# Kernel tuning notes

Hardware: AMD Instinct MI355X
Metric: run time of the kernel (lower is better)

The kernel has to match this reference:

```python
import jax, jax.numpy as jnp
import numpy as np

N_NODES = 200000
N_EDGES = 6400000
N_GRAPHS = 512
DIM_IN = 128
HID = 32
BN_EPS = 1e-5


def _gin(x, src, dst, w1, b1, w2, b2):
    # GINConv with eps=0: MLP(x + sum_{j in N(i)} x_j)
    agg = jax.ops.segment_sum(x[src], dst, num_segments=N_NODES)
    h = x + agg
    h = jnp.maximum(h @ w1 + b1, 0.0)
    return h @ w2 + b2


def _bn(x, gamma, beta):
    # BatchNorm1d, training mode: batch stats, biased variance
    m = jnp.mean(x, axis=0)
    v = jnp.var(x, axis=0)
    return gamma * (x - m) * jax.lax.rsqrt(v + BN_EPS) + beta


def setup_inputs() -> dict:
    key = jax.random.key(0)
    ks = jax.random.split(key, 20)
    s = 0.1
    inp = {
        "x": jax.random.normal(ks[0], (N_NODES, DIM_IN), jnp.float32),
        "edge_index": jax.random.randint(ks[1], (2, N_EDGES), 0, N_NODES, jnp.int32),
        "batch": jnp.sort(jax.random.randint(ks[2], (N_NODES,), 0, N_GRAPHS, jnp.int32)),
        "e0_w1": s * jax.random.normal(ks[3], (DIM_IN, HID), jnp.float32),
        "e0_b1": s * jax.random.normal(ks[4], (HID,), jnp.float32),
        "e0_w2": s * jax.random.normal(ks[5], (HID, HID), jnp.float32),
        "e0_b2": s * jax.random.normal(ks[6], (HID,), jnp.float32),
        "enc_w1": s * jax.random.normal(ks[7], (4, HID, HID), jnp.float32),
        "enc_b1": s * jax.random.normal(ks[8], (4, HID), jnp.float32),
        "enc_w2": s * jax.random.normal(ks[9], (4, HID, HID), jnp.float32),
        "enc_b2": s * jax.random.normal(ks[10], (4, HID), jnp.float32),
        "enc_gamma": jnp.ones((5, HID), jnp.float32),
        "enc_beta": jnp.zeros((5, HID), jnp.float32),
        "dec_w1": s * jax.random.normal(ks[11], (5, HID, HID), jnp.float32),
        "dec_b1": s * jax.random.normal(ks[12], (5, HID), jnp.float32),
        "dec_w2": s * jax.random.normal(ks[13], (4, HID, HID), jnp.float32),
        "dec_b2": s * jax.random.normal(ks[14], (4, HID), jnp.float32),
        "dec_w2_last": s * jax.random.normal(ks[15], (HID, DIM_IN), jnp.float32),
        "dec_b2_last": s * jax.random.normal(ks[16], (DIM_IN,), jnp.float32),
        "dec_gamma": jnp.ones((4, HID), jnp.float32),
        "dec_beta": jnp.zeros((4, HID), jnp.float32),
    }
    return inp


def reference(x, edge_index, batch,
              e0_w1, e0_b1, e0_w2, e0_b2,
              enc_w1, enc_b1, enc_w2, enc_b2, enc_gamma, enc_beta,
              dec_w1, dec_b1, dec_w2, dec_b2, dec_w2_last, dec_b2_last,
              dec_gamma, dec_beta):
    src, dst = edge_index[0], edge_index[1]

    # ----- Encoder: 5 GIN layers, ReLU then BN, collect per-layer reps -----
    xs = []
    h = jnp.maximum(_gin(x, src, dst, e0_w1, e0_b1, e0_w2, e0_b2), 0.0)
    h = _bn(h, enc_gamma[0], enc_beta[0])
    xs.append(h)
    for i in range(4):
        h = jnp.maximum(_gin(h, src, dst, enc_w1[i], enc_b1[i], enc_w2[i], enc_b2[i]), 0.0)
        h = _bn(h, enc_gamma[i + 1], enc_beta[i + 1])
        xs.append(h)
    encoded_rep = h

    # ----- Decoder: 5 GIN layers, ReLU; BN on all but last -----
    d = encoded_rep
    for i in range(5):
        w2 = dec_w2[i] if i < 4 else dec_w2_last
        b2 = dec_b2[i] if i < 4 else dec_b2_last
        d = jnp.maximum(_gin(d, src, dst, dec_w1[i], dec_b1[i], w2, b2), 0.0)
        if i < 4:
            d = _bn(d, dec_gamma[i], dec_beta[i])
    decoded_rep = d

    # ----- Global add pool of each encoder layer output, concat -----
    xpool = [jax.ops.segment_sum(xi, batch, num_segments=N_GRAPHS) for xi in xs]
    global_rep = jnp.concatenate(xpool, axis=1)  # [G, 5*32]

    return encoded_rep, decoded_rep, global_rep
```

## Files before the change

kernel.cpp:

```cpp
#include <hip/hip_runtime.h>
#include <hip/hip_bf16.h>
#include <hip/hip_fp16.h>
#include <string.h>

#define N_NODES  200000
#define N_EDGES  6400000
#define N_GRAPHS 512
#define DIM_IN   128
#define HID      32
#define BN_EPS   1e-5f

#define CHUNK    2048
#define NCHUNKS  98

typedef const float* fp;

__device__ __forceinline__ unsigned short f2h(float f) {
    __half h = __float2half(f);
    unsigned short u; __builtin_memcpy(&u, &h, 2); return u;
}
__device__ __forceinline__ float2 h2f2(unsigned int u) {
    __half2 h; __builtin_memcpy(&h, &u, 4);
    return __half22float2(h);
}


__global__ __launch_bounds__(256) void k_hist2(const int* __restrict__ dst,
                                               int* __restrict__ deg) {
    __shared__ int lh[12500];
    const int grp = blockIdx.x & 15;
    const int blk = blockIdx.x >> 4;
    const int lo = grp * 12500;
    for (int j = threadIdx.x; j < 12500; j += 256) lh[j] = 0;
    __syncthreads();
    const int4* d4 = reinterpret_cast<const int4*>(dst) + blk * 50000;
    for (int j = threadIdx.x; j < 12500; j += 256) {
        int4 v0 = d4[j];
        int4 v1 = d4[j + 12500];
        int4 v2 = d4[j + 25000];
        int4 v3 = d4[j + 37500];
        int a;
        a = v0.x - lo; if ((unsigned)a < 12500u) atomicAdd(&lh[a], 1);
        a = v0.y - lo; if ((unsigned)a < 12500u) atomicAdd(&lh[a], 1);
        a = v0.z - lo; if ((unsigned)a < 12500u) atomicAdd(&lh[a], 1);
        a = v0.w - lo; if ((unsigned)a < 12500u) atomicAdd(&lh[a], 1);
        a = v1.x - lo; if ((unsigned)a < 12500u) atomicAdd(&lh[a], 1);
        a = v1.y - lo; if ((unsigned)a < 12500u) atomicAdd(&lh[a], 1);
        a = v1.z - lo; if ((unsigned)a < 12500u) atomicAdd(&lh[a], 1);
        a = v1.w - lo; if ((unsigned)a < 12500u) atomicAdd(&lh[a], 1);
        a = v2.x - lo; if ((unsigned)a < 12500u) atomicAdd(&lh[a], 1);
        a = v2.y - lo; if ((unsigned)a < 12500u) atomicAdd(&lh[a], 1);
        a = v2.z - lo; if ((unsigned)a < 12500u) atomicAdd(&lh[a], 1);
        a = v2.w - lo; if ((unsigned)a < 12500u) atomicAdd(&lh[a], 1);
        a = v3.x - lo; if ((unsigned)a < 12500u) atomicAdd(&lh[a], 1);
        a = v3.y - lo; if ((unsigned)a < 12500u) atomicAdd(&lh[a], 1);
        a = v3.z - lo; if ((unsigned)a < 12500u) atomicAdd(&lh[a], 1);
        a = v3.w - lo; if ((unsigned)a < 12500u) atomicAdd(&lh[a], 1);
    }
    __syncthreads();
    for (int j = threadIdx.x; j < 12500; j += 256) {
        int c = lh[j];
        if (c) atomicAdd(&deg[lo + j], c);
    }
}

__global__ void k_chunksum(const int* __restrict__ deg, int* __restrict__ chunksum) {
    __shared__ int red[256];
    int b = blockIdx.x, t = threadIdx.x;
    int base = b * CHUNK;
    int s = 0;
    for (int k = 0; k < 8; ++k) {
        int i = base + t + k * 256;
        if (i < N_NODES) s += deg[i];
    }
    red[t] = s; __syncthreads();
    for (int off = 128; off > 0; off >>= 1) {
        if (t < off) red[t] += red[t + off];
        __syncthreads();
    }
    if (t == 0) chunksum[b] = red[0];
}

__global__ void k_scanchunks(const int* __restrict__ chunksum, int* __restrict__ chunkoff,
                             int* __restrict__ rowptr) {
    __shared__ int buf[128];
    int t = threadIdx.x;
    int v = (t < NCHUNKS) ? chunksum[t] : 0;
    buf[t] = v; __syncthreads();
    for (int off = 1; off < 128; off <<= 1) {
        int add = (t >= off) ? buf[t - off] : 0;
        __syncthreads();
        buf[t] += add;
        __syncthreads();
    }
    if (t < NCHUNKS) chunkoff[t] = buf[t] - v;
    if (t == 0) rowptr[N_NODES] = N_EDGES;
}

__global__ void k_scanfinal(const int* __restrict__ deg, const int* __restrict__ chunkoff,
                            int* __restrict__ rowptr, int* __restrict__ fillpos) {
    __shared__ int tsum[256];
    int b = blockIdx.x, t = threadIdx.x;
    int base = b * CHUNK + t * 8;
    int v[8]; int s = 0;
    for (int k = 0; k < 8; ++k) {
        int i = base + k;
        v[k] = (i < N_NODES) ? deg[i] : 0;
        s += v[k];
    }
    tsum[t] = s; __syncthreads();
    for (int off = 1; off < 256; off <<= 1) {
        int add = (t >= off) ? tsum[t - off] : 0;
        __syncthreads();
        tsum[t] += add;
        __syncthreads();
    }
    int run = tsum[t] - s + chunkoff[b];
    for (int k = 0; k < 8; ++k) {
        int i = base + k;
        if (i < N_NODES) { rowptr[i] = run; fillpos[i] = run; run += v[k]; }
    }
}

__global__ __launch_bounds__(256) void k_fill2(
    const int* __restrict__ src, const int* __restrict__ dst,
    int* __restrict__ fillpos, int* __restrict__ csr, int blk0)
{
    const int grp = blockIdx.x & 7;
    const int blk = blk0 + (blockIdx.x >> 3);
    const int lo = grp * 25000, hi = lo + 25000;
    const int4* d4 = reinterpret_cast<const int4*>(dst) + blk * 3125;
    const int4* s4 = reinterpret_cast<const int4*>(src) + blk * 3125;
    for (int j = threadIdx.x; j < 3125; j += 256) {
        int4 d = d4[j];
        int4 s = s4[j];
        if (d.x >= lo && d.x < hi) { int p = atomicAdd(&fillpos[d.x], 1); csr[p] = s.x; }
        if (d.y >= lo && d.y < hi) { int p = atomicAdd(&fillpos[d.y], 1); csr[p] = s.y; }
        if (d.z >= lo && d.z < hi) { int p = atomicAdd(&fillpos[d.z], 1); csr[p] = s.z; }
        if (d.w >= lo && d.w < hi) { int p = atomicAdd(&fillpos[d.w], 1); csr[p] = s.w; }
    }
}

__global__ void k_bounds(const int* __restrict__ batch, int* __restrict__ gstart) {
    int g = blockIdx.x * blockDim.x + threadIdx.x;
    if (g > N_GRAPHS) return;
    if (g == N_GRAPHS) { gstart[g] = N_NODES; return; }
    int lo = 0, hi = N_NODES;
    while (lo < hi) {
        int mid = (lo + hi) >> 1;
        if (batch[mid] < g) lo = mid + 1; else hi = mid;
    }
    gstart[g] = lo;
}


__global__ __launch_bounds__(256) void k_proj128(
    const float* __restrict__ x, fp w1, float* __restrict__ y,
    unsigned short* __restrict__ y16)
{
    __shared__ float w1s[DIM_IN * 32];
    for (int i = threadIdx.x; i < DIM_IN * 32; i += 256) w1s[i] = w1[i];
    __syncthreads();
    const int lane = threadIdx.x & 63;
    const int c = lane & 31;
    const int srcBase = lane & 32;
    int worker   = (blockIdx.x * blockDim.x + threadIdx.x) >> 5;
    int nworkers = (gridDim.x * blockDim.x) >> 5;
    for (int n = worker; n < N_NODES; n += nworkers) {
        const float* xr = x + (size_t)n * DIM_IN;
        float x0 = xr[c], x1 = xr[32 + c], x2 = xr[64 + c], x3 = xr[96 + c];
        float acc = 0.f;
        #pragma unroll
        for (int k = 0; k < 32; ++k) {
            acc = fmaf(__shfl(x0, srcBase | k, 64), w1s[k * 32 + c], acc);
            acc = fmaf(__shfl(x1, srcBase | k, 64), w1s[(32 + k) * 32 + c], acc);
            acc = fmaf(__shfl(x2, srcBase | k, 64), w1s[(64 + k) * 32 + c], acc);
            acc = fmaf(__shfl(x3, srcBase | k, 64), w1s[(96 + k) * 32 + c], acc);
        }
        y[(size_t)n * 32 + c] = acc;
        y16[(size_t)n * 32 + c] = f2h(acc);
    }
}


__global__ __launch_bounds__(256) void k_gather8(
    const float* __restrict__ h, const unsigned short* __restrict__ h16,
    const int* __restrict__ rowptr, const int* __restrict__ csr,
    float* __restrict__ sout,
    const float* __restrict__ stats, fp gamma, fp beta)
{
    const int lane = threadIdx.x & 63;
    const int sub  = lane & 15;
    const int q    = sub & 7;
    const int hh   = sub >> 3;
    const int srcBase = lane & 48;
    float sc0 = 1.f, sc1 = 1.f, sc2 = 1.f, sc3 = 1.f;
    float sh0 = 0.f, sh1 = 0.f, sh2 = 0.f, sh3 = 0.f;
    if (stats) {
        const int c0 = 4 * q;
        float m0 = stats[c0 + 0] * (1.f / N_NODES);
        float m1 = stats[c0 + 1] * (1.f / N_NODES);
        float m2 = stats[c0 + 2] * (1.f / N_NODES);
        float m3 = stats[c0 + 3] * (1.f / N_NODES);
        float v0 = stats[32 + c0 + 0] * (1.f / N_NODES) - m0 * m0;
        float v1 = stats[32 + c0 + 1] * (1.f / N_NODES) - m1 * m1;
        float v2 = stats[32 + c0 + 2] * (1.f / N_NODES) - m2 * m2;
        float v3 = stats[32 + c0 + 3] * (1.f / N_NODES) - m3 * m3;
        sc0 = gamma[c0 + 0] * rsqrtf(v0 + BN_EPS);
        sc1 = gamma[c0 + 1] * rsqrtf(v1 + BN_EPS);
        sc2 = gamma[c0 + 2] * rsqrtf(v2 + BN_EPS);
        sc3 = gamma[c0 + 3] * rsqrtf(v3 + BN_EPS);
        sh0 = beta[c0 + 0] - m0 * sc0;
        sh1 = beta[c0 + 1] - m1 * sc1;
        sh2 = beta[c0 + 2] - m2 * sc2;
        sh3 = beta[c0 + 3] - m3 * sc3;
    }
    const uint2*  hp2 = reinterpret_cast<const uint2*>(h16);
    const float4* hs4 = reinterpret_cast<const float4*>(h);
    float4* so4 = reinterpret_cast<float4*>(sout);
    int worker   = (blockIdx.x * blockDim.x + threadIdx.x) >> 4;
    int nworkers = (gridDim.x * blockDim.x) >> 4;
    for (int n = worker; n < N_NODES; n += nworkers) {
        int e0 = rowptr[n], e1 = rowptr[n + 1];
        float a0 = 0.f, a1 = 0.f, a2 = 0.f, a3 = 0.f;
        int e = e0;
        while (e < e1) {
            int rem = e1 - e;
            int cnt = rem < 16 ? rem : 16;
            int myidx = (sub < cnt) ? csr[e + sub] : 0;
            if (cnt == 16) {
                int i0 = __shfl(myidx, srcBase | (0  + hh), 64);
                int i1 = __shfl(myidx, srcBase | (2  + hh), 64);
                int i2 = __shfl(myidx, srcBase | (4  + hh), 64);
                int i3 = __shfl(myidx, srcBase | (6  + hh), 64);
                int i4 = __shfl(myidx, srcBase | (8  + hh), 64);
                int i5 = __shfl(myidx, srcBase | (10 + hh), 64);
                int i6 = __shfl(myidx, srcBase | (12 + hh), 64);
                int i7 = __shfl(myidx, srcBase | (14 + hh), 64);
                uint2 u0 = hp2[(size_t)i0 * 8 + q];
                uint2 u1 = hp2[(size_t)i1 * 8 + q];
                uint2 u2 = hp2[(size_t)i2 * 8 + q];
                uint2 u3 = hp2[(size_t)i3 * 8 + q];
                uint2 u4 = hp2[(size_t)i4 * 8 + q];
                uint2 u5 = hp2[(size_t)i5 * 8 + q];
                uint2 u6 = hp2[(size_t)i6 * 8 + q];
                uint2 u7 = hp2[(size_t)i7 * 8 + q];
                float2 fA, fB;
                fA = h2f2(u0.x); fB = h2f2(u0.y);
                a0 += fA.x; a1 += fA.y; a2 += fB.x; a3 += fB.y;
                fA = h2f2(u1.x); fB = h2f2(u1.y);
                a0 += fA.x; a1 += fA.y; a2 += fB.x; a3 += fB.y;
                fA = h2f2(u2.x); fB = h2f2(u2.y);
                a0 += fA.x; a1 += fA.y; a2 += fB.x; a3 += fB.y;
                fA = h2f2(u3.x); fB = h2f2(u3.y);
                a0 += fA.x; a1 += fA.y; a2 += fB.x; a3 += fB.y;
                fA = h2f2(u4.x); fB = h2f2(u4.y);
                a0 += fA.x; a1 += fA.y; a2 += fB.x; a3 += fB.y;
                fA = h2f2(u5.x); fB = h2f2(u5.y);
                a0 += fA.x; a1 += fA.y; a2 += fB.x; a3 += fB.y;
                fA = h2f2(u6.x); fB = h2f2(u6.y);
                a0 += fA.x; a1 += fA.y; a2 += fB.x; a3 += fB.y;
                fA = h2f2(u7.x); fB = h2f2(u7.y);
                a0 += fA.x; a1 += fA.y; a2 += fB.x; a3 += fB.y;
            } else {
                int k = 0;
                for (; k + 2 <= cnt; k += 2) {
                    int i = __shfl(myidx, srcBase | (k + hh), 64);
                    uint2 u = hp2[(size_t)i * 8 + q];
                    float2 fA = h2f2(u.x), fB = h2f2(u.y);
                    a0 += fA.x; a1 += fA.y; a2 += fB.x; a3 += fB.y;
                }
                if (k < cnt) {
                    int i = __shfl(myidx, srcBase | k, 64);
                    if (hh == 0) {
                        uint2 u = hp2[(size_t)i * 8 + q];
                        float2 fA = h2f2(u.x), fB = h2f2(u.y);
                        a0 += fA.x; a1 += fA.y; a2 += fB.x; a3 += fB.y;
                    }
                }
            }
            e += cnt;
        }
        a0 += __shfl_xor(a0, 8, 64);
        a1 += __shfl_xor(a1, 8, 64);
        a2 += __shfl_xor(a2, 8, 64);
        a3 += __shfl_xor(a3, 8, 64);
        float4 self = hs4[(size_t)n * 8 + q];
        float dc = (float)(e1 - e0 + 1);
        float4 o;
        o.x = fmaf(a0 + self.x, sc0, dc * sh0);
        o.y = fmaf(a1 + self.y, sc1, dc * sh1);
        o.z = fmaf(a2 + self.z, sc2, dc * sh2);
        o.w = fmaf(a3 + self.w, sc3, dc * sh3);
        if (hh == 0) so4[(size_t)n * 8 + q] = o;
    }
}


__global__ __launch_bounds__(256) void k_mlp32(
    const float* __restrict__ s, fp w1, fp b1, fp w2, fp b2,
    float* __restrict__ hout, unsigned short* __restrict__ h16out,
    float* __restrict__ stats)
{
    const int lane = threadIdx.x & 63;
    const int c = lane & 31;
    const int srcBase = lane & 32;
    float w1r[32], w2r[32];
    #pragma unroll
    for (int k = 0; k < 32; ++k) {
        w1r[k] = w1[k * 32 + c];
        w2r[k] = w2[k * 32 + c];
    }
    const float b1c = b1[c];
    const float b2c = b2[c];
    int worker   = (blockIdx.x * blockDim.x + threadIdx.x) >> 5;
    int nworkers = (gridDim.x * blockDim.x) >> 5;
    float s1 = 0.f, s2 = 0.f;
    for (int n = worker; n < N_NODES; n += nworkers) {
        float sv = s[(size_t)n * 32 + c];
        float acc1 = b1c;
        #pragma unroll
        for (int k = 0; k < 32; ++k)
            acc1 = fmaf(__shfl(sv, srcBase | k, 64), w1r[k], acc1);
        float h3 = fmaxf(acc1, 0.f);
        float acc2 = b2c;
        #pragma unroll
        for (int k = 0; k < 32; ++k)
            acc2 = fmaf(__shfl(h3, srcBase | k, 64), w2r[k], acc2);
        float a = fmaxf(acc2, 0.f);
        hout[(size_t)n * 32 + c] = a;
        h16out[(size_t)n * 32 + c] = f2h(a);
        s1 += a; s2 += a * a;
    }
    s1 += __shfl_xor(s1, 32, 64);
    s2 += __shfl_xor(s2, 32, 64);
    __shared__ float ls1[4][32], ls2[4][32];
    int w = threadIdx.x >> 6;
    if ((threadIdx.x & 32) == 0) { ls1[w][c] = s1; ls2[w][c] = s2; }
    __syncthreads();
    if (threadIdx.x < 32) {
        float t1 = ls1[0][c] + ls1[1][c] + ls1[2][c] + ls1[3][c];
        float t2 = ls2[0][c] + ls2[1][c] + ls2[2][c] + ls2[3][c];
        atomicAdd(&stats[c], t1);
        atomicAdd(&stats[32 + c], t2);
    }
}

__global__ __launch_bounds__(256) void k_mlp0(
    const float* __restrict__ s, fp b1, fp w2, fp b2,
    float* __restrict__ hout, unsigned short* __restrict__ h16out,
    float* __restrict__ stats)
{
    const int lane = threadIdx.x & 63;
    const int c = lane & 31;
    const int srcBase = lane & 32;
    float w2r[32];
    #pragma unroll
    for (int k = 0; k < 32; ++k) w2r[k] = w2[k * 32 + c];
    const float b1c = b1[c];
    const float b2c = b2[c];
    int worker   = (blockIdx.x * blockDim.x + threadIdx.x) >> 5;
    int nworkers = (gridDim.x * blockDim.x) >> 5;
    float s1 = 0.f, s2 = 0.f;
    for (int n = worker; n < N_NODES; n += nworkers) {
        float sv = s[(size_t)n * 32 + c];
        float h3 = fmaxf(sv + b1c, 0.f);
        float acc2 = b2c;
        #pragma unroll
        for (int k = 0; k < 32; ++k)
            acc2 = fmaf(__shfl(h3, srcBase | k, 64), w2r[k], acc2);
        float a = fmaxf(acc2, 0.f);
        hout[(size_t)n * 32 + c] = a;
        h16out[(size_t)n * 32 + c] = f2h(a);
        s1 += a; s2 += a * a;
    }
    s1 += __shfl_xor(s1, 32, 64);
    s2 += __shfl_xor(s2, 32, 64);
    __shared__ float ls1[4][32], ls2[4][32];
    int w = threadIdx.x >> 6;
    if ((threadIdx.x & 32) == 0) { ls1[w][c] = s1; ls2[w][c] = s2; }
    __syncthreads();
    if (threadIdx.x < 32) {
        float t1 = ls1[0][c] + ls1[1][c] + ls1[2][c] + ls1[3][c];
        float t2 = ls2[0][c] + ls2[1][c] + ls2[2][c] + ls2[3][c];
        atomicAdd(&stats[c], t1);
        atomicAdd(&stats[32 + c], t2);
    }
}

__global__ __launch_bounds__(256) void k_mlp_last(
    const float* __restrict__ s, fp w1, fp b1, fp w2 , fp b2,
    float* __restrict__ out)
{
    const int lane = threadIdx.x & 63;
    const int c = lane & 31;
    float w1r[32], w2a[32], w2b[32];
    #pragma unroll
    for (int k = 0; k < 32; ++k) {
        w1r[k] = w1[k * 32 + c];
        w2a[k] = w2[k * 128 + 2 * lane];
        w2b[k] = w2[k * 128 + 2 * lane + 1];
    }
    const float b1c = b1[c];
    const float b2a = b2[2 * lane];
    const float b2b = b2[2 * lane + 1];
    int worker   = (blockIdx.x * blockDim.x + threadIdx.x) >> 6;
    int nworkers = (gridDim.x * blockDim.x) >> 6;
    for (int n = worker; n < N_NODES; n += nworkers) {
        float sv = s[(size_t)n * 32 + c];
        float acc1 = b1c;
        #pragma unroll
        for (int k = 0; k < 32; ++k)
            acc1 = fmaf(__shfl(sv, k, 64), w1r[k], acc1);
        float h3 = fmaxf(acc1, 0.f);
        float oa = b2a, ob = b2b;
        #pragma unroll
        for (int k = 0; k < 32; ++k) {
            float v = __shfl(h3, (lane & 32) | k, 64);
            oa = fmaf(v, w2a[k], oa);
            ob = fmaf(v, w2b[k], ob);
        }
        oa = fmaxf(oa, 0.f); ob = fmaxf(ob, 0.f);
        float2 pr; pr.x = oa; pr.y = ob;
        reinterpret_cast<float2*>(out)[(size_t)n * 64 + lane] = pr;
    }
}

__global__ void k_bnout(const float* __restrict__ h, const float* __restrict__ stats,
                        fp gamma, fp beta, float* __restrict__ out)
{
    const int c = threadIdx.x & 31;
    float m  = stats[c] * (1.f / N_NODES);
    float vv = stats[32 + c] * (1.f / N_NODES) - m * m;
    float sc = gamma[c] * rsqrtf(vv + BN_EPS);
    float sh = beta[c] - m * sc;
    int i = blockIdx.x * blockDim.x + threadIdx.x;
    int stride = gridDim.x * blockDim.x;
    for (; i < N_NODES * 32; i += stride) out[i] = fmaf(h[i], sc, sh);
}

__global__ void k_pool(const float* __restrict__ h, const int* __restrict__ gstart,
                       float* __restrict__ out, int col0,
                       const float* __restrict__ stats, fp gamma, fp beta)
{
    int g = blockIdx.x;
    int t = threadIdx.x;
    int f = t & 31, j = t >> 5;
    int n0 = gstart[g], n1 = gstart[g + 1];
    float s = 0.f;
    for (int n = n0 + j; n < n1; n += 8) s += h[(size_t)n * 32 + f];
    __shared__ float red[8][32];
    red[j][f] = s; __syncthreads();
    if (t < 32) {
        float tot = 0.f;
        #pragma unroll
        for (int k = 0; k < 8; ++k) tot += red[k][f];
        float m  = stats[f] * (1.f / N_NODES);
        float vv = stats[32 + f] * (1.f / N_NODES) - m * m;
        float sc = gamma[f] * rsqrtf(vv + BN_EPS);
        float sh = beta[f] - m * sc;
        out[g * (5 * HID) + col0 + f] = fmaf(tot, sc, (float)(n1 - n0) * sh);
    }
}


extern "C" void kernel_launch(void* const* d_in, const int* in_sizes, int n_in,
                              void* d_out, int out_size, void* d_ws, size_t ws_size,
                              hipStream_t stream) {
    fp         x        = (fp)d_in[0];
    const int* edge     = (const int*)d_in[1];
    const int* batch    = (const int*)d_in[2];
    fp e0_w1 = (fp)d_in[3],  e0_b1 = (fp)d_in[4];
    fp e0_w2 = (fp)d_in[5],  e0_b2 = (fp)d_in[6];
    fp enc_w1 = (fp)d_in[7],  enc_b1 = (fp)d_in[8];
    fp enc_w2 = (fp)d_in[9],  enc_b2 = (fp)d_in[10];
    fp enc_gamma = (fp)d_in[11], enc_beta = (fp)d_in[12];
    fp dec_w1 = (fp)d_in[13], dec_b1 = (fp)d_in[14];
    fp dec_w2 = (fp)d_in[15], dec_b2 = (fp)d_in[16];
    fp dec_w2_last = (fp)d_in[17], dec_b2_last = (fp)d_in[18];
    fp dec_gamma = (fp)d_in[19], dec_beta = (fp)d_in[20];

    const int* srcp = edge;
    const int* dstp = edge + N_EDGES;

    float* out_enc    = (float*)d_out;
    float* out_dec    = (float*)d_out + (size_t)N_NODES * 32;
    float* out_global = (float*)d_out + (size_t)N_NODES * 160;

    char* p = (char*)d_ws;
    auto alloc = [&](size_t bytes) -> void* {
        void* r = (void*)p;
        p += (bytes + 255) & ~(size_t)255;
        return r;
    };
    int*   rowptr   = (int*)alloc((N_NODES + 1) * sizeof(int));
    int*   fillpos  = (int*)alloc(N_NODES * sizeof(int));
    int*   deg      = (int*)alloc(N_NODES * sizeof(int));
    int*   chunksum = (int*)alloc(128 * sizeof(int));
    int*   chunkoff = (int*)alloc(128 * sizeof(int));
    int*   gstart   = (int*)alloc((N_GRAPHS + 1) * sizeof(int));
    float* stats    = (float*)alloc(9 * 64 * sizeof(float));
    int*   csr      = (int*)alloc((size_t)N_EDGES * sizeof(int));
    float* hbuf     = (float*)alloc((size_t)N_NODES * 32 * sizeof(float));
    float* sbuf     = (float*)alloc((size_t)N_NODES * 32 * sizeof(float));
    unsigned short* h16 = (unsigned short*)alloc((size_t)N_NODES * 32 * sizeof(unsigned short));

    hipMemsetAsync(deg, 0, N_NODES * sizeof(int), stream);
    hipMemsetAsync(stats, 0, 9 * 64 * sizeof(float), stream);

    k_hist2<<<512, 256, 0, stream>>>(dstp, deg);
    k_chunksum<<<NCHUNKS, 256, 0, stream>>>(deg, chunksum);
    k_scanchunks<<<1, 128, 0, stream>>>(chunksum, chunkoff, rowptr);
    k_scanfinal<<<NCHUNKS, 256, 0, stream>>>(deg, chunkoff, rowptr, fillpos);
    k_fill2<<<2048, 256, 0, stream>>>(srcp, dstp, fillpos, csr, 0);
    k_fill2<<<2048, 256, 0, stream>>>(srcp, dstp, fillpos, csr, 256);
    k_bounds<<<3, 256, 0, stream>>>(batch, gstart);

    k_proj128<<<1024, 256, 0, stream>>>(x, e0_w1, hbuf, h16);
    k_gather8<<<2048, 256, 0, stream>>>(hbuf, h16, rowptr, csr, sbuf,
                                        nullptr, nullptr, nullptr);
    k_mlp0<<<1024, 256, 0, stream>>>(sbuf, e0_b1, e0_w2, e0_b2, hbuf, h16, stats);
    k_pool<<<N_GRAPHS, 256, 0, stream>>>(hbuf, gstart, out_global, 0,
                                         stats, enc_gamma, enc_beta);

    for (int i = 0; i < 4; ++i) {
        float* st_prev = stats + i * 64;
        float* st      = stats + (1 + i) * 64;
        k_gather8<<<2048, 256, 0, stream>>>(hbuf, h16, rowptr, csr, sbuf,
                                            st_prev, enc_gamma + i * 32, enc_beta + i * 32);
        k_mlp32<<<1024, 256, 0, stream>>>(sbuf,
                                          enc_w1 + i * 1024, enc_b1 + i * 32,
                                          enc_w2 + i * 1024, enc_b2 + i * 32,
                                          hbuf, h16, st);
        k_pool<<<N_GRAPHS, 256, 0, stream>>>(hbuf, gstart, out_global, (1 + i) * 32,
                                             st, enc_gamma + (1 + i) * 32,
                                             enc_beta + (1 + i) * 32);
    }

    k_bnout<<<2048, 256, 0, stream>>>(hbuf, stats + 4 * 64,
                                      enc_gamma + 4 * 32, enc_beta + 4 * 32, out_enc);

    for (int i = 0; i < 4; ++i) {
        float* st_prev = (i == 0) ? (stats + 4 * 64) : (stats + (4 + i) * 64);
        fp g_prev      = (i == 0) ? (enc_gamma + 4 * 32) : (dec_gamma + (i - 1) * 32);
        fp b_prev      = (i == 0) ? (enc_beta  + 4 * 32) : (dec_beta  + (i - 1) * 32);
        float* st      = stats + (5 + i) * 64;
        k_gather8<<<2048, 256, 0, stream>>>(hbuf, h16, rowptr, csr, sbuf,
                                            st_prev, g_prev, b_prev);
        k_mlp32<<<1024, 256, 0, stream>>>(sbuf,
                                          dec_w1 + i * 1024, dec_b1 + i * 32,
                                          dec_w2 + i * 1024, dec_b2 + i * 32,
                                          hbuf, h16, st);
    }

    k_gather8<<<2048, 256, 0, stream>>>(hbuf, h16, rowptr, csr, sbuf,
                                        stats + 8 * 64, dec_gamma + 3 * 32,
                                        dec_beta + 3 * 32);
    k_mlp_last<<<1024, 256, 0, stream>>>(sbuf,
                                         dec_w1 + 4 * 1024, dec_b1 + 4 * 32,
                                         dec_w2_last, dec_b2_last, out_dec);
}
```

Baseline: 2.754 ms.

## Read self term from fp16 buffer, merge fill launches, two nodes per proj worker

The gather kernel now takes each node's self feature from the fp16 copy already being gathered, instead of a separate fp32 load. This removes one 128-byte read per node per layer, at the cost of rounding the self term to half precision. The two fill launches are merged into a single 4096-block launch. The first projection now has each 32-lane worker process two nodes per iteration, so each shared-memory weight load is reused twice.

```diff
diff --git a/kernel.cpp b/kernel.cpp
--- a/kernel.cpp
+++ b/kernel.cpp
@@ -124,10 +124,10 @@
 
 __global__ __launch_bounds__(256) void k_fill2(
     const int* __restrict__ src, const int* __restrict__ dst,
-    int* __restrict__ fillpos, int* __restrict__ csr, int blk0)
+    int* __restrict__ fillpos, int* __restrict__ csr)
 {
     const int grp = blockIdx.x & 7;
-    const int blk = blk0 + (blockIdx.x >> 3);
+    const int blk = blockIdx.x >> 3;
     const int lo = grp * 25000, hi = lo + 25000;
     const int4* d4 = reinterpret_cast<const int4*>(dst) + blk * 3125;
     const int4* s4 = reinterpret_cast<const int4*>(src) + blk * 3125;
@@ -166,25 +166,37 @@
     const int srcBase = lane & 32;
     int worker   = (blockIdx.x * blockDim.x + threadIdx.x) >> 5;
     int nworkers = (gridDim.x * blockDim.x) >> 5;
-    for (int n = worker; n < N_NODES; n += nworkers) {
-        const float* xr = x + (size_t)n * DIM_IN;
-        float x0 = xr[c], x1 = xr[32 + c], x2 = xr[64 + c], x3 = xr[96 + c];
-        float acc = 0.f;
+    for (int n = 2 * worker; n < N_NODES; n += 2 * nworkers) {
+        const float* xa = x + (size_t)n * DIM_IN;
+        const float* xb = xa + DIM_IN;
+        float a0 = xa[c], a1 = xa[32 + c], a2 = xa[64 + c], a3 = xa[96 + c];
+        float b0 = xb[c], b1 = xb[32 + c], b2 = xb[64 + c], b3 = xb[96 + c];
+        float accA = 0.f, accB = 0.f;
         #pragma unroll
         for (int k = 0; k < 32; ++k) {
-            acc = fmaf(__shfl(x0, srcBase | k, 64), w1s[k * 32 + c], acc);
-            acc = fmaf(__shfl(x1, srcBase | k, 64), w1s[(32 + k) * 32 + c], acc);
-            acc = fmaf(__shfl(x2, srcBase | k, 64), w1s[(64 + k) * 32 + c], acc);
-            acc = fmaf(__shfl(x3, srcBase | k, 64), w1s[(96 + k) * 32 + c], acc);
+            float w0 = w1s[k * 32 + c];
+            float w1v = w1s[(32 + k) * 32 + c];
+            float w2v = w1s[(64 + k) * 32 + c];
+            float w3v = w1s[(96 + k) * 32 + c];
+            accA = fmaf(__shfl(a0, srcBase | k, 64), w0, accA);
+            accB = fmaf(__shfl(b0, srcBase | k, 64), w0, accB);
+            accA = fmaf(__shfl(a1, srcBase | k, 64), w1v, accA);
+            accB = fmaf(__shfl(b1, srcBase | k, 64), w1v, accB);
+            accA = fmaf(__shfl(a2, srcBase | k, 64), w2v, accA);
+            accB = fmaf(__shfl(b2, srcBase | k, 64), w2v, accB);
+            accA = fmaf(__shfl(a3, srcBase | k, 64), w3v, accA);
+            accB = fmaf(__shfl(b3, srcBase | k, 64), w3v, accB);
         }
-        y[(size_t)n * 32 + c] = acc;
-        y16[(size_t)n * 32 + c] = f2h(acc);
+        y[(size_t)n * 32 + c] = accA;
+        y16[(size_t)n * 32 + c] = f2h(accA);
+        y[(size_t)(n + 1) * 32 + c] = accB;
+        y16[(size_t)(n + 1) * 32 + c] = f2h(accB);
     }
 }
 
 
 __global__ __launch_bounds__(256) void k_gather8(
-    const float* __restrict__ h, const unsigned short* __restrict__ h16,
+    const unsigned short* __restrict__ h16,
     const int* __restrict__ rowptr, const int* __restrict__ csr,
     float* __restrict__ sout,
     const float* __restrict__ stats, fp gamma, fp beta)
@@ -215,14 +227,18 @@
         sh2 = beta[c0 + 2] - m2 * sc2;
         sh3 = beta[c0 + 3] - m3 * sc3;
     }
-    const uint2*  hp2 = reinterpret_cast<const uint2*>(h16);
-    const float4* hs4 = reinterpret_cast<const float4*>(h);
+    const uint2* hp2 = reinterpret_cast<const uint2*>(h16);
     float4* so4 = reinterpret_cast<float4*>(sout);
     int worker   = (blockIdx.x * blockDim.x + threadIdx.x) >> 4;
     int nworkers = (gridDim.x * blockDim.x) >> 4;
     for (int n = worker; n < N_NODES; n += nworkers) {
+        uint2 us = hp2[(size_t)n * 8 + q];
         int e0 = rowptr[n], e1 = rowptr[n + 1];
-        float a0 = 0.f, a1 = 0.f, a2 = 0.f, a3 = 0.f;
+        float2 sA = h2f2(us.x), sB = h2f2(us.y);
+        float a0 = (hh == 0) ? sA.x : 0.f;
+        float a1 = (hh == 0) ? sA.y : 0.f;
+        float a2 = (hh == 0) ? sB.x : 0.f;
+        float a3 = (hh == 0) ? sB.y : 0.f;
         int e = e0;
         while (e < e1) {
             int rem = e1 - e;
@@ -285,13 +301,12 @@
         a1 += __shfl_xor(a1, 8, 64);
         a2 += __shfl_xor(a2, 8, 64);
         a3 += __shfl_xor(a3, 8, 64);
-        float4 self = hs4[(size_t)n * 8 + q];
         float dc = (float)(e1 - e0 + 1);
         float4 o;
-        o.x = fmaf(a0 + self.x, sc0, dc * sh0);
-        o.y = fmaf(a1 + self.y, sc1, dc * sh1);
-        o.z = fmaf(a2 + self.z, sc2, dc * sh2);
-        o.w = fmaf(a3 + self.w, sc3, dc * sh3);
+        o.x = fmaf(a0, sc0, dc * sh0);
+        o.y = fmaf(a1, sc1, dc * sh1);
+        o.z = fmaf(a2, sc2, dc * sh2);
+        o.w = fmaf(a3, sc3, dc * sh3);
         if (hh == 0) so4[(size_t)n * 8 + q] = o;
     }
 }
@@ -512,12 +527,11 @@
     k_chunksum<<<NCHUNKS, 256, 0, stream>>>(deg, chunksum);
     k_scanchunks<<<1, 128, 0, stream>>>(chunksum, chunkoff, rowptr);
     k_scanfinal<<<NCHUNKS, 256, 0, stream>>>(deg, chunkoff, rowptr, fillpos);
-    k_fill2<<<2048, 256, 0, stream>>>(srcp, dstp, fillpos, csr, 0);
-    k_fill2<<<2048, 256, 0, stream>>>(srcp, dstp, fillpos, csr, 256);
+    k_fill2<<<4096, 256, 0, stream>>>(srcp, dstp, fillpos, csr);
     k_bounds<<<3, 256, 0, stream>>>(batch, gstart);
 
     k_proj128<<<1024, 256, 0, stream>>>(x, e0_w1, hbuf, h16);
-    k_gather8<<<2048, 256, 0, stream>>>(hbuf, h16, rowptr, csr, sbuf,
+    k_gather8<<<2048, 256, 0, stream>>>(h16, rowptr, csr, sbuf,
                                         nullptr, nullptr, nullptr);
     k_mlp0<<<1024, 256, 0, stream>>>(sbuf, e0_b1, e0_w2, e0_b2, hbuf, h16, stats);
     k_pool<<<N_GRAPHS, 256, 0, stream>>>(hbuf, gstart, out_global, 0,
@@ -526,7 +540,7 @@
     for (int i = 0; i < 4; ++i) {
         float* st_prev = stats + i * 64;
         float* st      = stats + (1 + i) * 64;
-        k_gather8<<<2048, 256, 0, stream>>>(hbuf, h16, rowptr, csr, sbuf,
+        k_gather8<<<2048, 256, 0, stream>>>(h16, rowptr, csr, sbuf,
                                             st_prev, enc_gamma + i * 32, enc_beta + i * 32);
         k_mlp32<<<1024, 256, 0, stream>>>(sbuf,
                                           enc_w1 + i * 1024, enc_b1 + i * 32,
@@ -545,7 +559,7 @@
         fp g_prev      = (i == 0) ? (enc_gamma + 4 * 32) : (dec_gamma + (i - 1) * 32);
         fp b_prev      = (i == 0) ? (enc_beta  + 4 * 32) : (dec_beta  + (i - 1) * 32);
         float* st      = stats + (5 + i) * 64;
-        k_gather8<<<2048, 256, 0, stream>>>(hbuf, h16, rowptr, csr, sbuf,
+        k_gather8<<<2048, 256, 0, stream>>>(h16, rowptr, csr, sbuf,
                                             st_prev, g_prev, b_prev);
         k_mlp32<<<1024, 256, 0, stream>>>(sbuf,
                                           dec_w1 + i * 1024, dec_b1 + i * 32,
@@ -553,7 +567,7 @@
                                           hbuf, h16, st);
     }
 
-    k_gather8<<<2048, 256, 0, stream>>>(hbuf, h16, rowptr, csr, sbuf,
+    k_gather8<<<2048, 256, 0, stream>>>(h16, rowptr, csr, sbuf,
                                         stats + 8 * 64, dec_gamma + 3 * 32,
                                         dec_beta + 3 * 32);
     k_mlp_last<<<1024, 256, 0, stream>>>(sbuf,
```

Result: faster. 2.678 ms (-2.8%).
